# Performance work log

Measured on AMD Instinct MI355X. Metric: run time of the kernel, lower is better.

## Reference

```python
import jax, jax.numpy as jnp
import numpy as np

N_EMBD = 2048
N_HEAD = 32
N_GROUPS = 8
HEAD_DIM = N_EMBD // N_HEAD
Q_PER_KV = N_HEAD // N_GROUPS
QKV_DIM = (Q_PER_KV + 2) * N_GROUPS * HEAD_DIM


def apply_rope(x, cos, sin):
    # x: [B, nH, T, hd]; cos/sin: [T, rot//2]
    B, nH, T, hd = x.shape
    rot = min(sin.shape[1] * 2, hd)
    half = rot // 2
    x_rot, x_pass = x[..., :rot], x[..., rot:]
    c = cos[:T, :half][None, None]  # [1,1,T,half]
    s = sin[:T, :half][None, None]
    x1, x2 = x_rot[..., :half], x_rot[..., half:]
    x1_ = x1 * c - x2 * s
    x2_ = x2 * c + x1 * s
    return jnp.concatenate([x1_, x2_, x_pass], axis=-1)


def setup_inputs() -> dict:
    key = jax.random.key(0)
    k1, k2, k3, k4, k5 = jax.random.split(key, 5)
    B, T = 2, 2048
    x = jax.random.normal(k1, (B, T, N_EMBD), dtype=jnp.float32)
    cos = jax.random.uniform(k2, (T, HEAD_DIM // 2), dtype=jnp.float32)
    sin = jax.random.uniform(k3, (T, HEAD_DIM // 2), dtype=jnp.float32)
    attn_w = jax.random.normal(k4, (QKV_DIM, N_EMBD), dtype=jnp.float32) * (1.0 / np.sqrt(N_EMBD))
    proj_w = jax.random.normal(k5, (N_EMBD, N_EMBD), dtype=jnp.float32) * (1.0 / np.sqrt(N_EMBD))
    return {"x": x, "cos": cos, "sin": sin, "attn_w": attn_w, "proj_w": proj_w}


def reference(x, cos, sin, attn_w, proj_w):
    B, T, E = x.shape
    qkv = jnp.einsum('bte,fe->btf', x, attn_w)  # [B,T,QKV_DIM]
    qkv = qkv.reshape(B, T, N_GROUPS, Q_PER_KV + 2, HEAD_DIM)
    q = qkv[:, :, :, :Q_PER_KV].reshape(B, T, N_HEAD, HEAD_DIM)
    k = qkv[:, :, :, Q_PER_KV]      # [B,T,G,hd]
    v = qkv[:, :, :, Q_PER_KV + 1]  # [B,T,G,hd]
    # [B, heads, T, hd] layout; GQA repeat_interleave of K/V to full head count
    q = q.transpose(0, 2, 1, 3)
    k = jnp.repeat(k.transpose(0, 2, 1, 3), Q_PER_KV, axis=1)
    v = jnp.repeat(v.transpose(0, 2, 1, 3), Q_PER_KV, axis=1)
    q = apply_rope(q, cos, sin)
    k = apply_rope(k, cos, sin)
    scale = 1.0 / np.sqrt(HEAD_DIM)
    att = jax.nn.softmax(jnp.einsum('bhqd,bhkd->bhqk', q, k) * scale, axis=-1)
    out = jnp.einsum('bhqk,bhkd->bhqd', att, v)  # [B,nH,T,hd]
    out = out.transpose(0, 2, 1, 3).reshape(B, T, N_HEAD * HEAD_DIM)
    return jnp.einsum('bte,fe->btf', out, proj_w)
```

## Files before the change

### kernel.cpp

```cpp
#include <hip/hip_runtime.h>

typedef unsigned short u16;
typedef unsigned int u32;
typedef __bf16 bf16x8 __attribute__((ext_vector_type(8)));
typedef float f32x4 __attribute__((ext_vector_type(4)));
typedef float f32x16 __attribute__((ext_vector_type(16)));
typedef unsigned int u32x4 __attribute__((ext_vector_type(4)));

__device__ __forceinline__ u16 f2bf(float f) {
    u32 u = __builtin_bit_cast(u32, f);
    u32 r = u + 0x7FFFu + ((u >> 16) & 1u);
    return (u16)(r >> 16);
}
__device__ __forceinline__ u32 pack_bf16(float v0, float v1) {
    u32 a = __builtin_bit_cast(u32, v0) + 0x8000u;
    u32 b = __builtin_bit_cast(u32, v1) + 0x8000u;
    return __builtin_amdgcn_perm(b, a, 0x07060302u);
}
__device__ __forceinline__ u32 cvtpk(float lo, float hi) {
    u32 r;
    asm("v_cvt_pk_bf16_f32 %0, %1, %2" : "=v"(r) : "v"(lo), "v"(hi));
    return r;
}
__device__ __forceinline__ void plswap(u32& a, u32& b) {
    asm("v_permlane32_swap_b32 %0, %1" : "+v"(a), "+v"(b));
}
__device__ __forceinline__ void gload16(const u16* g, u16* l) {
    __builtin_amdgcn_global_load_lds(
        (const __attribute__((address_space(1))) u32*)g,
        (__attribute__((address_space(3))) u32*)l, 16, 0, 0);
}

#define QSCALE 0.18033688011111793f


__global__ __launch_bounds__(256) void cvt3_kernel(const float* __restrict__ a, u16* __restrict__ ao,
                                                   const float* __restrict__ b, u16* __restrict__ bo,
                                                   const float* __restrict__ c, u16* __restrict__ co) {
    int i = blockIdx.x * 256 + threadIdx.x;
    const float* src; u16* dst; int idx;
    if (i < 2097152)       { src = a; dst = ao; idx = i; }
    else if (i < 3670016)  { src = b; dst = bo; idx = i - 2097152; }
    else                   { src = c; dst = co; idx = i - 3670016; }
    float4 f = reinterpret_cast<const float4*>(src)[idx];
    u32 lo = (u32)f2bf(f.x) | ((u32)f2bf(f.y) << 16);
    u32 hi = (u32)f2bf(f.z) | ((u32)f2bf(f.w) << 16);
    reinterpret_cast<uint2*>(dst)[idx] = make_uint2(lo, hi);
}

__global__ __launch_bounds__(512, 2) void gemm_qkv(const u16* __restrict__ A,
                                                   const u16* __restrict__ Bw,
                                                   const float* __restrict__ cosb,
                                                   const float* __restrict__ sinb,
                                                   u16* __restrict__ Qo,
                                                   u16* __restrict__ Ko,
                                                   u16* __restrict__ Vt) {
    __shared__ __align__(16) u16 As[2 * 2 * 128 * 64];
    __shared__ __align__(16) u16 Bs[2 * 2 * 128 * 64];
    const int tid = threadIdx.x;
    const int w = tid >> 6, lane = tid & 63;
    const int quad = lane >> 4, l15 = lane & 15;
    const int wr = w >> 2, wc = w & 3;
    const int m0 = blockIdx.x * 256, n0 = blockIdx.y * 256;
    const int K = 2048;
    const int rsub = lane >> 3;
    const int csrc = (lane & 7) ^ rsub;
    const int sx = (l15 & 7) << 3;
    const int c0 = (quad * 8) ^ sx;
    const int c1 = (32 + quad * 8) ^ sx;

    f32x4 acc[8][4];
#pragma unroll
    for (int a = 0; a < 8; a++)
#pragma unroll
        for (int b = 0; b < 4; b++) acc[a][b] = (f32x4){0.f, 0.f, 0.f, 0.f};

    auto stage = [&](const u16* g, int row0, int kk, u16* lds) {
#pragma unroll
        for (int i = 0; i < 2; i++)
            gload16(g + (size_t)(row0 + (i * 8 + w) * 8 + rsub) * K + kk + csrc * 8,
                    lds + (i * 8 + w) * 512);
    };

    stage(A,  m0,       0, &As[0]);
    stage(A,  m0 + 128, 0, &As[8192]);
    stage(Bw, n0,       0, &Bs[0]);
    stage(Bw, n0 + 128, 0, &Bs[8192]);
    asm volatile("s_waitcnt vmcnt(0)" ::: "memory");
    __builtin_amdgcn_s_barrier();

    for (int j = 0; j < 32; ++j) {
        const int cur = j & 1;
        const u16* Ab = &As[cur * 16384 + wr * 8192];
        const u16* Bb = &Bs[cur * 16384 + (wc >> 1) * 8192 + (wc & 1) * 4096];
        u16* Asn = &As[(cur ^ 1) * 16384];
        u16* Bsn = &Bs[(cur ^ 1) * 16384];
        const int kk2 = (j + 1) * 64;
        bf16x8 af[4][2];
#pragma unroll
        for (int q = 0; q < 4; ++q) {
            const int qm = q >> 1, qn = q & 1;
            if (qn == 0) {
#pragma unroll
                for (int fm = 0; fm < 4; fm++) {
                    af[fm][0] = *reinterpret_cast<const bf16x8*>(&Ab[(qm * 64 + fm * 16 + l15) * 64 + c0]);
                    af[fm][1] = *reinterpret_cast<const bf16x8*>(&Ab[(qm * 64 + fm * 16 + l15) * 64 + c1]);
                }
            }
            bf16x8 bfv[2][2];
#pragma unroll
            for (int fn = 0; fn < 2; fn++) {
                bfv[fn][0] = *reinterpret_cast<const bf16x8*>(&Bb[(qn * 32 + fn * 16 + l15) * 64 + c0]);
                bfv[fn][1] = *reinterpret_cast<const bf16x8*>(&Bb[(qn * 32 + fn * 16 + l15) * 64 + c1]);
            }
            if (j < 31) {
                if (q == 0)      { stage(A,  m0,       kk2, Asn); stage(A,  m0 + 128, kk2, Asn + 8192); }
                else if (q == 1) { stage(Bw, n0,       kk2, Bsn); stage(Bw, n0 + 128, kk2, Bsn + 8192); }
            }
            __builtin_amdgcn_s_barrier();
            __builtin_amdgcn_s_setprio(1);
#pragma unroll
            for (int fm = 0; fm < 4; fm++)
#pragma unroll
                for (int fn = 0; fn < 2; fn++) {
                    acc[qm * 4 + fm][qn * 2 + fn] = __builtin_amdgcn_mfma_f32_16x16x32_bf16(
                        af[fm][0], bfv[fn][0], acc[qm * 4 + fm][qn * 2 + fn], 0, 0, 0);
                    acc[qm * 4 + fm][qn * 2 + fn] = __builtin_amdgcn_mfma_f32_16x16x32_bf16(
                        af[fm][1], bfv[fn][1], acc[qm * 4 + fm][qn * 2 + fn], 0, 0, 0);
                }
            __builtin_amdgcn_s_setprio(0);
            if (q == 3 && j < 31) asm volatile("s_waitcnt vmcnt(0)" ::: "memory");
            __builtin_amdgcn_s_barrier();
        }
    }

    const int nw0 = n0 + wc * 64;
    const int G = nw0 / 384;
    const int slot = (nw0 % 384) / 64;
    const int bb = m0 >> 11;
    const int tb0 = (m0 & 2047) + wr * 128 + quad * 4;
    if (slot == 5) {
        u16* vbase = Vt + ((size_t)(bb * 8 + G)) * 131072;
        const int half_v = quad >> 1, jb = (quad & 1) * 4;
#pragma unroll
        for (int fm = 0; fm < 8; fm++) {
            const int trow = tb0 + fm * 16;
            const int sb = (trow >> 6) * 4096 + ((trow >> 4) & 3) * 512 + half_v * 256 + jb;
#pragma unroll
            for (int fn = 0; fn < 4; fn++) {
                const int dt = fn >> 1, dl = (fn & 1) * 16 + l15;
                uint2 pk;
                pk.x = pack_bf16(acc[fm][fn][0], acc[fm][fn][1]);
                pk.y = pack_bf16(acc[fm][fn][2], acc[fm][fn][3]);
                *reinterpret_cast<uint2*>(vbase + sb + dt * 2048 + dl * 8) = pk;
            }
        }
    } else {
        const float sc = (slot < 4) ? QSCALE : 1.0f;
        u16* obase = (slot < 4)
            ? Qo + ((size_t)(bb * 32 + G * 4 + slot)) * 131072
            : Ko + ((size_t)(bb * 8 + G)) * 131072;
        const int laneoff = (l15 >> 3) * 256 + (l15 & 7);
#pragma unroll
        for (int fm = 0; fm < 8; fm++) {
#pragma unroll
            for (int i = 0; i < 4; i++) {
                const int t = tb0 + fm * 16 + i;
                const int tb = (t >> 5) * 2048 + (t & 31) * 8 + laneoff;
#pragma unroll
                for (int fn = 0; fn < 2; fn++) {
                    const int dh = fn * 16 + l15;
                    float c = cosb[t * 32 + dh], s = sinb[t * 32 + dh];
                    float x1 = acc[fm][fn][i], x2 = acc[fm][fn + 2][i];
                    obase[tb + fn * 512]       = f2bf((x1 * c - x2 * s) * sc);
                    obase[tb + (fn + 2) * 512] = f2bf((x2 * c + x1 * s) * sc);
                }
            }
        }
    }
}

__global__ __launch_bounds__(512, 2) void gemm_bt(const u16* __restrict__ A,
                                                  const u16* __restrict__ Bw,
                                                  float* __restrict__ Cf,
                                                  int M, int N, int K) {
    __shared__ __align__(16) u16 As[2 * 128 * 64];
    __shared__ __align__(16) u16 Bs[2 * 2 * 128 * 64];
    const int tid = threadIdx.x;
    const int w = tid >> 6, lane = tid & 63;
    const int quad = lane >> 4, l15 = lane & 15;
    const int wr = w >> 2, wc = w & 3;
    const int m0 = blockIdx.x * 128, n0 = blockIdx.y * 256;
    const int rsub = lane >> 3;
    const int csrc = (lane & 7) ^ rsub;
    const int sx = (l15 & 7) << 3;
    const int c0 = (quad * 8) ^ sx;
    const int c1 = (32 + quad * 8) ^ sx;

    f32x4 acc[4][4];
#pragma unroll
    for (int a = 0; a < 4; a++)
#pragma unroll
        for (int b = 0; b < 4; b++) acc[a][b] = (f32x4){0.f, 0.f, 0.f, 0.f};

    auto stage = [&](const u16* g, int row0, int kk, u16* lds) {
#pragma unroll
        for (int i = 0; i < 2; i++)
            gload16(g + (size_t)(row0 + (i * 8 + w) * 8 + rsub) * K + kk + csrc * 8,
                    lds + (i * 8 + w) * 512);
    };

    stage(A,  m0,       0, &As[0]);
    stage(Bw, n0,       0, &Bs[0]);
    stage(Bw, n0 + 128, 0, &Bs[8192]);
    asm volatile("s_waitcnt vmcnt(0)" ::: "memory");
    __builtin_amdgcn_s_barrier();

    const int nt = K >> 6;
    for (int j = 0; j < nt; ++j) {
        const int cur = j & 1;
        const u16* Ab = &As[cur * 8192];
        const u16* Bb = &Bs[cur * 16384 + (wc >> 1) * 8192 + (wc & 1) * 4096];
        u16* Asn = &As[(cur ^ 1) * 8192];
        u16* Bsn = &Bs[(cur ^ 1) * 16384];
        const int kk2 = (j + 1) * 64;
        bf16x8 af[2][2];
#pragma unroll
        for (int q = 0; q < 4; ++q) {
            const int qm = q >> 1, qn = q & 1;
            if (qn == 0) {
#pragma unroll
                for (int fm = 0; fm < 2; fm++) {
                    const int r = wr * 64 + (qm * 2 + fm) * 16 + l15;
                    af[fm][0] = *reinterpret_cast<const bf16x8*>(&Ab[r * 64 + c0]);
                    af[fm][1] = *reinterpret_cast<const bf16x8*>(&Ab[r * 64 + c1]);
                }
            }
            bf16x8 bfv[2][2];
#pragma unroll
            for (int fn = 0; fn < 2; fn++) {
                bfv[fn][0] = *reinterpret_cast<const bf16x8*>(&Bb[(qn * 32 + fn * 16 + l15) * 64 + c0]);
                bfv[fn][1] = *reinterpret_cast<const bf16x8*>(&Bb[(qn * 32 + fn * 16 + l15) * 64 + c1]);
            }
            if (j < nt - 1) {
                if (q == 0)      stage(A,  m0, kk2, Asn);
                else if (q == 1) { stage(Bw, n0, kk2, Bsn); stage(Bw, n0 + 128, kk2, Bsn + 8192); }
            }
            __builtin_amdgcn_s_barrier();
            __builtin_amdgcn_s_setprio(1);
#pragma unroll
            for (int fm = 0; fm < 2; fm++)
#pragma unroll
                for (int fn = 0; fn < 2; fn++) {
                    acc[qm * 2 + fm][qn * 2 + fn] = __builtin_amdgcn_mfma_f32_16x16x32_bf16(
                        af[fm][0], bfv[fn][0], acc[qm * 2 + fm][qn * 2 + fn], 0, 0, 0);
                    acc[qm * 2 + fm][qn * 2 + fn] = __builtin_amdgcn_mfma_f32_16x16x32_bf16(
                        af[fm][1], bfv[fn][1], acc[qm * 2 + fm][qn * 2 + fn], 0, 0, 0);
                }
            __builtin_amdgcn_s_setprio(0);
            if (q == 3 && j < nt - 1) asm volatile("s_waitcnt vmcnt(0)" ::: "memory");
            __builtin_amdgcn_s_barrier();
        }
    }

#pragma unroll
    for (int tm = 0; tm < 4; tm++) {
        const int r0 = m0 + wr * 64 + tm * 16 + quad * 4;
#pragma unroll
        for (int tn = 0; tn < 4; tn++) {
            const int c = n0 + wc * 64 + tn * 16 + l15;
#pragma unroll
            for (int i = 0; i < 4; i++) Cf[(size_t)(r0 + i) * N + c] = acc[tm][tn][i];
        }
    }
}

__global__ __launch_bounds__(256, 4) void attn(const u16* __restrict__ Q,
                                               const u16* __restrict__ Kg,
                                               const u16* __restrict__ Vt,
                                               u16* __restrict__ O) {
    __shared__ __align__(16) u16 Ks[3 * 4096];
    __shared__ __align__(16) u16 Vts[2 * 4096];
    const int tid = threadIdx.x, w = tid >> 6, lane = tid & 63;
    const int half = lane >> 5, l31 = lane & 31;
    const int q0 = blockIdx.x * 128;
    const int h = blockIdx.y, b = blockIdx.z, g = h >> 2;
    const u16* qfb = Q + ((size_t)(b * 32 + h)) * 131072;
    const u16* kfb = Kg + ((size_t)(b * 8 + g)) * 131072;
    const u16* vfb = Vt + ((size_t)(b * 8 + g)) * 131072;

    const int Tq = (q0 >> 6) + (w >> 1);
#pragma unroll
    for (int ks = 0; ks < 4; ks++)
        gload16(qfb + ((size_t)((Tq * 8 + (w & 1) * 4 + ks) * 64) + lane) * 8,
                Ks + (w * 4 + ks) * 512);
    __syncthreads();
    bf16x8 qf[4];
#pragma unroll
    for (int ks = 0; ks < 4; ks++)
        qf[ks] = *reinterpret_cast<const bf16x8*>(&Ks[(w * 4 + ks) * 512 + lane * 8]);
    __syncthreads();

    f32x16 Oa[2];
#pragma unroll
    for (int t = 0; t < 2; t++)
#pragma unroll
        for (int i = 0; i < 16; i++) Oa[t][i] = 0.f;
    float lsum = 0.f;

    auto stage_k = [&](int T, int bsel) {
        u16* kd = Ks + bsel * 4096;
#pragma unroll
        for (int i = 0; i < 2; i++) {
            const int s = w * 2 + i;
            gload16(kfb + ((size_t)((T * 8 + s) * 64) + lane) * 8, kd + s * 512);
        }
    };
    auto stage_v = [&](int T, int bsel) {
        u16* vd = Vts + bsel * 4096;
#pragma unroll
        for (int i = 0; i < 2; i++) {
            const int s = w * 2 + i;
            gload16(vfb + ((size_t)((T * 8 + s) * 64) + lane) * 8, vd + s * 512);
        }
    };
    auto qk = [&](f32x16 (&S)[2], const u16* Kb) {
#pragma unroll
        for (int kt = 0; kt < 2; kt++) {
#pragma unroll
            for (int i = 0; i < 16; i++) S[kt][i] = 0.f;
#pragma unroll
            for (int ks = 0; ks < 4; ks++) {
                bf16x8 kf = *reinterpret_cast<const bf16x8*>(&Kb[(kt * 4 + ks) * 512 + lane * 8]);
                S[kt] = __builtin_amdgcn_mfma_f32_32x32x16_bf16(kf, qf[ks], S[kt], 0, 0, 0);
            }
        }
    };

    stage_k(0, 0);
    stage_v(0, 0);
    stage_k(1, 1);
    __syncthreads();
    f32x16 Sa[2], Sb[2];
    __builtin_amdgcn_s_setprio(1);
    qk(Sa, Ks);
    __builtin_amdgcn_s_setprio(0);

    auto body = [&](int t, int bn, int bs, f32x16 (&Sc)[2], f32x16 (&Sn)[2],
                    const u16* Vb) {
        if (t < 31) stage_v(t + 1, (t + 1) & 1);
        if (t < 30) stage_k(t + 2, bs);
        float ps = 0.f;
        u32 pw[4][4];
#pragma unroll
        for (int kt = 0; kt < 2; kt++) {
            float pe[16];
#pragma unroll
            for (int r = 0; r < 16; r++) pe[r] = __builtin_amdgcn_exp2f(Sc[kt][r]);
#pragma unroll
            for (int r = 0; r < 4; r++)
                ps += (pe[r * 4 + 0] + pe[r * 4 + 1]) + (pe[r * 4 + 2] + pe[r * 4 + 3]);
#pragma unroll
            for (int j = 0; j < 2; j++) {
                u32 X0 = cvtpk(pe[j * 8 + 0], pe[j * 8 + 1]);
                u32 Y0 = cvtpk(pe[j * 8 + 4], pe[j * 8 + 5]);
                u32 X1 = cvtpk(pe[j * 8 + 2], pe[j * 8 + 3]);
                u32 Y1 = cvtpk(pe[j * 8 + 6], pe[j * 8 + 7]);
                plswap(X0, Y0);
                plswap(X1, Y1);
                const int ks2 = kt * 2 + j;
                pw[ks2][0] = X0; pw[ks2][1] = X1; pw[ks2][2] = Y0; pw[ks2][3] = Y1;
            }
        }
        __builtin_amdgcn_s_setprio(1);
        qk(Sn, Ks + bn * 4096);
#pragma unroll
        for (int ks2 = 0; ks2 < 4; ks2++) {
            u32x4 pv = (u32x4){pw[ks2][0], pw[ks2][1], pw[ks2][2], pw[ks2][3]};
            bf16x8 pf = __builtin_bit_cast(bf16x8, pv);
#pragma unroll
            for (int dt = 0; dt < 2; dt++) {
                bf16x8 vf = *reinterpret_cast<const bf16x8*>(
                    &Vb[(dt * 4 + ks2) * 512 + lane * 8]);
                Oa[dt] = __builtin_amdgcn_mfma_f32_32x32x16_bf16(vf, pf, Oa[dt], 0, 0, 0);
            }
        }
        __builtin_amdgcn_s_setprio(0);
        lsum += ps;
        __syncthreads();
    };

    int b0 = 0, b1 = 1, b2 = 2;
    for (int k2 = 0; k2 < 16; ++k2) {
        const int t0 = k2 * 2;
        body(t0,     b1, b2, Sa, Sb, Vts);
        body(t0 + 1, b2, b0, Sb, Sa, Vts + 4096);
        const int nb0 = b2, nb1 = b0, nb2 = b1;
        b0 = nb0; b1 = nb1; b2 = nb2;
    }

    float lt = lsum + __shfl_xor(lsum, 32);
    float linv = 1.f / lt;
    const int t = q0 + w * 32 + l31;
    u16* orow = O + ((size_t)(b * 2048 + t)) * 2048 + h * 64;
#pragma unroll
    for (int dt = 0; dt < 2; dt++)
#pragma unroll
        for (int gr = 0; gr < 4; gr++) {
            uint2 pk;
            pk.x = pack_bf16(Oa[dt][gr * 4 + 0] * linv, Oa[dt][gr * 4 + 1] * linv);
            pk.y = pack_bf16(Oa[dt][gr * 4 + 2] * linv, Oa[dt][gr * 4 + 3] * linv);
            *reinterpret_cast<uint2*>(orow + dt * 32 + 8 * gr + 4 * half) = pk;
        }
}

extern "C" void kernel_launch(void* const* d_in, const int* in_sizes, int n_in,
                              void* d_out, int out_size, void* d_ws, size_t ws_size,
                              hipStream_t stream) {
    const float* x      = (const float*)d_in[0];
    const float* cosb   = (const float*)d_in[1];
    const float* sinb   = (const float*)d_in[2];
    const float* attn_w = (const float*)d_in[3];
    const float* proj_w = (const float*)d_in[4];
    float* out = (float*)d_out;

    u16* xb  = (u16*)d_ws;
    u16* w1b = xb  + (size_t)4096 * 2048;
    u16* w2b = w1b + (size_t)3072 * 2048;
    u16* qo  = w2b + (size_t)2048 * 2048;
    u16* ko  = qo  + (size_t)2 * 32 * 2048 * 64;
    u16* vt  = ko  + (size_t)2 * 8 * 2048 * 64;
    u16* ao  = xb;

    cvt3_kernel<<<18432, 256, 0, stream>>>(x, xb, attn_w, w1b, proj_w, w2b);
    gemm_qkv<<<dim3(16, 12), 512, 0, stream>>>(xb, w1b, cosb, sinb, qo, ko, vt);
    attn<<<dim3(16, 32, 2), 256, 0, stream>>>(qo, ko, vt, ao);
    gemm_bt<<<dim3(32, 8), 512, 0, stream>>>(ao, w2b, out, 4096, 2048, 2048);
}
```

Before: 311.3 us.

## Retile QKV GEMM to 128x384 blocks aligned with one KV group

Changes the QKV projection GEMM tile from 256x256 to 128x384, so each block covers exactly one KV group (4 Q heads, K, V). The grid goes from 192 to 256 blocks, and the warp layout becomes 4x2 with 32x192 per warp. The epilogue is reorganised per 64-column slot, and group/slot indexing now comes straight from blockIdx. This gives more blocks to fill the CUs, at the cost of a less square tile with lower A reuse and more B traffic per block.

```diff
diff --git a/kernel.cpp b/kernel.cpp
--- a/kernel.cpp
+++ b/kernel.cpp
@@ -55,13 +55,13 @@
                                                    u16* __restrict__ Qo,
                                                    u16* __restrict__ Ko,
                                                    u16* __restrict__ Vt) {
-    __shared__ __align__(16) u16 As[2 * 2 * 128 * 64];
-    __shared__ __align__(16) u16 Bs[2 * 2 * 128 * 64];
+    __shared__ __align__(16) u16 As[2 * 128 * 64];
+    __shared__ __align__(16) u16 Bs[2 * 384 * 64];
     const int tid = threadIdx.x;
     const int w = tid >> 6, lane = tid & 63;
     const int quad = lane >> 4, l15 = lane & 15;
-    const int wr = w >> 2, wc = w & 3;
-    const int m0 = blockIdx.x * 256, n0 = blockIdx.y * 256;
+    const int wr = w >> 1, wc = w & 1;
+    const int m0 = blockIdx.x * 128, n0 = blockIdx.y * 384;
     const int K = 2048;
     const int rsub = lane >> 3;
     const int csrc = (lane & 7) ^ rsub;
@@ -69,113 +69,117 @@
     const int c0 = (quad * 8) ^ sx;
     const int c1 = (32 + quad * 8) ^ sx;
 
-    f32x4 acc[8][4];
-#pragma unroll
-    for (int a = 0; a < 8; a++)
-#pragma unroll
-        for (int b = 0; b < 4; b++) acc[a][b] = (f32x4){0.f, 0.f, 0.f, 0.f};
-
-    auto stage = [&](const u16* g, int row0, int kk, u16* lds) {
+    f32x4 acc[2][12];
+#pragma unroll
+    for (int a = 0; a < 2; a++)
+#pragma unroll
+        for (int b = 0; b < 12; b++) acc[a][b] = (f32x4){0.f, 0.f, 0.f, 0.f};
+
+    auto stageA = [&](int kk, u16* lds) {
 #pragma unroll
         for (int i = 0; i < 2; i++)
-            gload16(g + (size_t)(row0 + (i * 8 + w) * 8 + rsub) * K + kk + csrc * 8,
+            gload16(A + (size_t)(m0 + (i * 8 + w) * 8 + rsub) * K + kk + csrc * 8,
                     lds + (i * 8 + w) * 512);
     };
-
-    stage(A,  m0,       0, &As[0]);
-    stage(A,  m0 + 128, 0, &As[8192]);
-    stage(Bw, n0,       0, &Bs[0]);
-    stage(Bw, n0 + 128, 0, &Bs[8192]);
+    auto stageB = [&](int kk, u16* lds, int hf) {
+#pragma unroll
+        for (int i = 0; i < 3; i++) {
+            const int grp = hf * 24 + i * 8 + w;
+            gload16(Bw + (size_t)(n0 + grp * 8 + rsub) * K + kk + csrc * 8,
+                    lds + grp * 512);
+        }
+    };
+
+    stageA(0, &As[0]);
+    stageB(0, &Bs[0], 0);
+    stageB(0, &Bs[0], 1);
     asm volatile("s_waitcnt vmcnt(0)" ::: "memory");
     __builtin_amdgcn_s_barrier();
 
     for (int j = 0; j < 32; ++j) {
         const int cur = j & 1;
-        const u16* Ab = &As[cur * 16384 + wr * 8192];
-        const u16* Bb = &Bs[cur * 16384 + (wc >> 1) * 8192 + (wc & 1) * 4096];
-        u16* Asn = &As[(cur ^ 1) * 16384];
-        u16* Bsn = &Bs[(cur ^ 1) * 16384];
+        const u16* Ab = &As[cur * 8192];
+        const u16* Bb = &Bs[cur * 24576];
+        u16* Asn = &As[(cur ^ 1) * 8192];
+        u16* Bsn = &Bs[(cur ^ 1) * 24576];
         const int kk2 = (j + 1) * 64;
-        bf16x8 af[4][2];
-#pragma unroll
-        for (int q = 0; q < 4; ++q) {
-            const int qm = q >> 1, qn = q & 1;
-            if (qn == 0) {
-#pragma unroll
-                for (int fm = 0; fm < 4; fm++) {
-                    af[fm][0] = *reinterpret_cast<const bf16x8*>(&Ab[(qm * 64 + fm * 16 + l15) * 64 + c0]);
-                    af[fm][1] = *reinterpret_cast<const bf16x8*>(&Ab[(qm * 64 + fm * 16 + l15) * 64 + c1]);
+        bf16x8 af[2][2];
+#pragma unroll
+        for (int ph = 0; ph < 2; ++ph) {
+            if (ph == 0) {
+#pragma unroll
+                for (int fm = 0; fm < 2; fm++) {
+                    const int r = wr * 32 + fm * 16 + l15;
+                    af[fm][0] = *reinterpret_cast<const bf16x8*>(&Ab[r * 64 + c0]);
+                    af[fm][1] = *reinterpret_cast<const bf16x8*>(&Ab[r * 64 + c1]);
                 }
             }
-            bf16x8 bfv[2][2];
-#pragma unroll
-            for (int fn = 0; fn < 2; fn++) {
-                bfv[fn][0] = *reinterpret_cast<const bf16x8*>(&Bb[(qn * 32 + fn * 16 + l15) * 64 + c0]);
-                bfv[fn][1] = *reinterpret_cast<const bf16x8*>(&Bb[(qn * 32 + fn * 16 + l15) * 64 + c1]);
+            bf16x8 bfv[6][2];
+#pragma unroll
+            for (int fn = 0; fn < 6; fn++) {
+                const int nr = wc * 192 + ph * 96 + fn * 16 + l15;
+                bfv[fn][0] = *reinterpret_cast<const bf16x8*>(&Bb[nr * 64 + c0]);
+                bfv[fn][1] = *reinterpret_cast<const bf16x8*>(&Bb[nr * 64 + c1]);
             }
             if (j < 31) {
-                if (q == 0)      { stage(A,  m0,       kk2, Asn); stage(A,  m0 + 128, kk2, Asn + 8192); }
-                else if (q == 1) { stage(Bw, n0,       kk2, Bsn); stage(Bw, n0 + 128, kk2, Bsn + 8192); }
+                if (ph == 0) { stageA(kk2, Asn); stageB(kk2, Bsn, 0); }
+                else         stageB(kk2, Bsn, 1);
             }
             __builtin_amdgcn_s_barrier();
             __builtin_amdgcn_s_setprio(1);
 #pragma unroll
-            for (int fm = 0; fm < 4; fm++)
-#pragma unroll
-                for (int fn = 0; fn < 2; fn++) {
-                    acc[qm * 4 + fm][qn * 2 + fn] = __builtin_amdgcn_mfma_f32_16x16x32_bf16(
-                        af[fm][0], bfv[fn][0], acc[qm * 4 + fm][qn * 2 + fn], 0, 0, 0);
-                    acc[qm * 4 + fm][qn * 2 + fn] = __builtin_amdgcn_mfma_f32_16x16x32_bf16(
-                        af[fm][1], bfv[fn][1], acc[qm * 4 + fm][qn * 2 + fn], 0, 0, 0);
+            for (int fm = 0; fm < 2; fm++)
+#pragma unroll
+                for (int fn = 0; fn < 6; fn++) {
+                    acc[fm][ph * 6 + fn] = __builtin_amdgcn_mfma_f32_16x16x32_bf16(
+                        af[fm][0], bfv[fn][0], acc[fm][ph * 6 + fn], 0, 0, 0);
+                    acc[fm][ph * 6 + fn] = __builtin_amdgcn_mfma_f32_16x16x32_bf16(
+                        af[fm][1], bfv[fn][1], acc[fm][ph * 6 + fn], 0, 0, 0);
                 }
             __builtin_amdgcn_s_setprio(0);
-            if (q == 3 && j < 31) asm volatile("s_waitcnt vmcnt(0)" ::: "memory");
+            if (ph == 1 && j < 31) asm volatile("s_waitcnt vmcnt(0)" ::: "memory");
             __builtin_amdgcn_s_barrier();
         }
     }
 
-    const int nw0 = n0 + wc * 64;
-    const int G = nw0 / 384;
-    const int slot = (nw0 % 384) / 64;
+    const int G = blockIdx.y;
     const int bb = m0 >> 11;
-    const int tb0 = (m0 & 2047) + wr * 128 + quad * 4;
-    if (slot == 5) {
-        u16* vbase = Vt + ((size_t)(bb * 8 + G)) * 131072;
-        const int half_v = quad >> 1, jb = (quad & 1) * 4;
-#pragma unroll
-        for (int fm = 0; fm < 8; fm++) {
-            const int trow = tb0 + fm * 16;
-            const int sb = (trow >> 6) * 4096 + ((trow >> 4) & 3) * 512 + half_v * 256 + jb;
-#pragma unroll
-            for (int fn = 0; fn < 4; fn++) {
-                const int dt = fn >> 1, dl = (fn & 1) * 16 + l15;
+    const int tb0 = (m0 & 2047) + wr * 32 + quad * 4;
+    const int laneoff = (l15 >> 3) * 256 + (l15 & 7);
+    u16* vbase = Vt + ((size_t)(bb * 8 + G)) * 131072;
+#pragma unroll
+    for (int fn = 0; fn < 12; fn++) {
+        const int slotf = wc * 3 + (fn >> 2);
+        const int f = fn & 3;
+        if (slotf == 5) {
+#pragma unroll
+            for (int fm = 0; fm < 2; fm++) {
+                const int trow = tb0 + fm * 16;
+                const int sb = (trow >> 6) * 4096 + ((trow >> 4) & 3) * 512
+                             + (quad >> 1) * 256 + (quad & 1) * 4;
                 uint2 pk;
                 pk.x = pack_bf16(acc[fm][fn][0], acc[fm][fn][1]);
                 pk.y = pack_bf16(acc[fm][fn][2], acc[fm][fn][3]);
-                *reinterpret_cast<uint2*>(vbase + sb + dt * 2048 + dl * 8) = pk;
-            }
-        }
-    } else {
-        const float sc = (slot < 4) ? QSCALE : 1.0f;
-        u16* obase = (slot < 4)
-            ? Qo + ((size_t)(bb * 32 + G * 4 + slot)) * 131072
-            : Ko + ((size_t)(bb * 8 + G)) * 131072;
-        const int laneoff = (l15 >> 3) * 256 + (l15 & 7);
-#pragma unroll
-        for (int fm = 0; fm < 8; fm++) {
-#pragma unroll
-            for (int i = 0; i < 4; i++) {
-                const int t = tb0 + fm * 16 + i;
-                const int tb = (t >> 5) * 2048 + (t & 31) * 8 + laneoff;
-#pragma unroll
-                for (int fn = 0; fn < 2; fn++) {
-                    const int dh = fn * 16 + l15;
+                *reinterpret_cast<uint2*>(vbase + sb + (f >> 1) * 2048
+                                          + ((f & 1) * 16 + l15) * 8) = pk;
+            }
+        } else if (f < 2) {
+            const float sc = (slotf < 4) ? QSCALE : 1.0f;
+            u16* obase = (slotf < 4)
+                ? Qo + ((size_t)(bb * 32 + G * 4 + slotf)) * 131072
+                : Ko + ((size_t)(bb * 8 + G)) * 131072;
+#pragma unroll
+            for (int fm = 0; fm < 2; fm++)
+#pragma unroll
+                for (int i = 0; i < 4; i++) {
+                    const int t = tb0 + fm * 16 + i;
+                    const int tb = (t >> 5) * 2048 + (t & 31) * 8 + laneoff;
+                    const int dh = f * 16 + l15;
                     float c = cosb[t * 32 + dh], s = sinb[t * 32 + dh];
                     float x1 = acc[fm][fn][i], x2 = acc[fm][fn + 2][i];
-                    obase[tb + fn * 512]       = f2bf((x1 * c - x2 * s) * sc);
-                    obase[tb + (fn + 2) * 512] = f2bf((x2 * c + x1 * s) * sc);
+                    obase[tb + f * 512]       = f2bf((x1 * c - x2 * s) * sc);
+                    obase[tb + (f + 2) * 512] = f2bf((x2 * c + x1 * s) * sc);
                 }
-            }
         }
     }
 }
@@ -433,7 +437,7 @@
     u16* ao  = xb;
 
     cvt3_kernel<<<18432, 256, 0, stream>>>(x, xb, attn_w, w1b, proj_w, w2b);
-    gemm_qkv<<<dim3(16, 12), 512, 0, stream>>>(xb, w1b, cosb, sinb, qo, ko, vt);
+    gemm_qkv<<<dim3(32, 8), 512, 0, stream>>>(xb, w1b, cosb, sinb, qo, ko, vt);
     attn<<<dim3(16, 32, 2), 256, 0, stream>>>(qo, ko, vt, ao);
     gemm_bt<<<dim3(32, 8), 512, 0, stream>>>(ao, w2b, out, 4096, 2048, 2048);
 }
```

After: 293.4 us. 5.8% less time.
